# Optimization experiments

Measured on AMD Instinct MI355X. Metric: run time of the kernel, lower is better.

The kernel has to match this reference:

```python
import jax, jax.numpy as jnp
import numpy as np

B, T, C, H, W = 4, 5, 512, 32, 32   # bt = B*T = 20
G = 32                              # GroupNorm groups
EPS = 1e-6


def group_norm(x, gamma, beta):
    # x: [N, C, H, W]; normalize per (group-channels, H, W)
    n, c, h, w = x.shape
    xg = x.reshape(n, G, c // G, h * w)
    mu = jnp.mean(xg, axis=(2, 3), keepdims=True)
    var = jnp.mean((xg - mu) ** 2, axis=(2, 3), keepdims=True)
    xn = ((xg - mu) * jax.lax.rsqrt(var + EPS)).reshape(n, c, h, w)
    return xn * gamma[None, :, None, None] + beta[None, :, None, None]


def conv1x1(x, w, b):
    # 1x1 conv == channel matmul. x: [N,C,H,W], w: [O,C], b: [O]
    return jnp.einsum('nchw,oc->nohw', x, w) + b[None, :, None, None]


def setup_inputs() -> dict:
    key = jax.random.key(0)
    ks = jax.random.split(key, 9)
    inp = {'x': jax.random.normal(ks[0], (B * T, C, H, W), jnp.float32)}
    for i, nm in enumerate(['wq', 'wk', 'wv', 'wo', 'wqt', 'wkt', 'wvt', 'wot']):
        inp[nm] = jax.random.normal(ks[i + 1], (C, C), jnp.float32) * 0.02
        inp['b' + nm[1:]] = jnp.zeros((C,), jnp.float32)
    inp['gamma_s'] = jnp.ones((C,), jnp.float32)
    inp['beta_s'] = jnp.zeros((C,), jnp.float32)
    inp['gamma_t'] = jnp.ones((C,), jnp.float32)
    inp['beta_t'] = jnp.zeros((C,), jnp.float32)
    return inp


def reference(x, wq, bq, wk, bk, wv, bv, wo, bo,
              wqt, bqt, wkt, bkt, wvt, bvt, wot, bot,
              gamma_s, beta_s, gamma_t, beta_t):
    scale = float(C) ** -0.5

    # ---- spatial attention (AttnBlock.forward) ----
    hn = group_norm(x, gamma_s, beta_s)
    q = conv1x1(hn, wq, bq).reshape(B * T, C, H * W)
    k = conv1x1(hn, wk, bk).reshape(B * T, C, H * W)
    v = conv1x1(hn, wv, bv).reshape(B * T, C, H * W)
    # scores [bt, hw_q, hw_k], softmax over keys
    att = jax.nn.softmax(jnp.einsum('bcq,bck->bqk', q, k) * scale, axis=2)
    hsp = jnp.einsum('bck,bqk->bcq', v, att).reshape(B * T, C, H, W)
    spatio = x + conv1x1(hsp, wo, bo)

    # ---- temporal attention across t=5 frames per pixel ----
    hn = group_norm(spatio, gamma_t, beta_t)
    q5 = conv1x1(hn, wqt, bqt).reshape(B, T, C, H, W)
    k5 = conv1x1(hn, wkt, bkt).reshape(B, T, C, H, W)
    v5 = conv1x1(hn, wvt, bvt).reshape(B, T, C, H, W)
    # per-pixel [t, t] attention, softmax over key-frame axis s
    att_t = jax.nn.softmax(jnp.einsum('btchw,bschw->bhwts', q5, k5) * scale, axis=-1)
    htp = jnp.einsum('bhwts,bschw->btchw', att_t, v5).reshape(B * T, C, H, W)

    # NOTE: residual is the ORIGINAL x (faithful to the source), not spatio
    return x + conv1x1(htp, wot, bot)
```

## Files before the change

### kernel.cpp

```cpp
#include <hip/hip_runtime.h>
#include <hip/hip_bf16.h>
#include <stdint.h>

typedef unsigned short u16;
typedef __attribute__((ext_vector_type(8))) short bf16x8;
typedef __attribute__((ext_vector_type(4))) float f32x4;

#define DI __device__ __forceinline__

DI float b2f(u16 u) { return __uint_as_float(((uint32_t)u) << 16); }
DI u16 f2b(float f) {
  uint32_t u = __float_as_uint(f);
  u += 0x7fff + ((u >> 16) & 1);
  return (u16)(u >> 16);
}

DI void gld_lds16(const u16* g, u16* l) {
  __builtin_amdgcn_global_load_lds((const __attribute__((address_space(1))) void*)g,
                                   (__attribute__((address_space(3))) void*)l,
                                   16, 0, 0);
}

__global__ __launch_bounds__(256)
void setup_wb(const float* __restrict__ w0, const float* __restrict__ w1,
              const float* __restrict__ w2, const float* __restrict__ w3,
              const float* __restrict__ w4, const float* __restrict__ w5,
              const float* __restrict__ w6, const float* __restrict__ w7,
              const float* __restrict__ b0, const float* __restrict__ b1,
              const float* __restrict__ b2, const float* __restrict__ b3,
              const float* __restrict__ b4, const float* __restrict__ b5,
              const float* __restrict__ b6, const float* __restrict__ b7,
              u16* __restrict__ dst, float* __restrict__ bdst)
{
  if (blockIdx.x >= 1032) {
    const int a = (blockIdx.x - 1032) * 256 + threadIdx.x;
    float acc = 0.f;
    for (int c = 0; c < 512; ++c) acc += w3[a * 512 + c] * b2[c];
    bdst[4096 + a] = acc;
    return;
  }
  if (blockIdx.x >= 1024) {
    const float* bs[8] = {b0, b1, b2, b3, b4, b5, b6, b7};
    const int a = blockIdx.x - 1024;
    const int i = threadIdx.x;
    bdst[a * 512 + i] = bs[a][i];
    bdst[a * 512 + i + 256] = bs[a][i + 256];
    return;
  }
  const float* srcs[8] = {w0, w1, w2, w3, w4, w5, w6, w7};
  const int mat = blockIdx.x >> 7;
  const int i = (((blockIdx.x & 127) << 8) + threadIdx.x) * 8;
  const float* s = srcs[mat];
  float4 a = *(const float4*)(s + i);
  float4 b = *(const float4*)(s + i + 4);
  alignas(16) u16 v[8] = {f2b(a.x), f2b(a.y), f2b(a.z), f2b(a.w),
                          f2b(b.x), f2b(b.y), f2b(b.z), f2b(b.w)};
  *(uint4*)(dst + (long)mat * 262144 + i) = *(const uint4*)v;
  if (mat == 2) {
    const int row = i >> 9, col = i & 511;
#pragma unroll
    for (int j = 0; j < 8; ++j) dst[8 * 262144 + (col + j) * 512 + row] = v[j];
  }
}

template<int OUTF32, int BIASMODE, int RESID, int SMEXP, int COLSCALE>
__global__ __launch_bounds__(256)
void gemm_bt(const u16* __restrict__ A, long sA, long lda,
             const u16* __restrict__ B, long sB, long ldb,
             void* __restrict__ C, long sC,
             const float* __restrict__ bias,
             const float* __restrict__ resid, long sR,
             int N, int K, float alpha, float* __restrict__ stats)
{
  __shared__ u16 lA[2 * 128 * 32];
  __shared__ u16 lB[2 * 128 * 32];
  const int t = threadIdx.x;
  const int lane = t & 63;
  const int wid = t >> 6;

  const int nx = gridDim.x;
  const int bid = blockIdx.y * nx + blockIdx.x;
  const int nper = (nx * gridDim.y) >> 3;
  const int nid = (bid & 7) * nper + (bid >> 3);
  const int m0 = (nid / nx) * 128, n0 = (nid % nx) * 128;

  const long bz = blockIdx.z;
  const u16* Ab = A + bz * sA;
  const u16* Bb = B + bz * sB;

  const int row = t >> 2;
  const int kc  = (((t & 3) ^ ((t >> 3) & 3)) << 3);

  f32x4 acc[4][4];
#pragma unroll
  for (int i = 0; i < 4; ++i)
#pragma unroll
    for (int j = 0; j < 4; ++j) acc[i][j] = (f32x4){0.f, 0.f, 0.f, 0.f};

  const int ml = lane & 15, qd = lane >> 4;
  const int koff = ((qd ^ ((ml >> 1) & 3)) << 3);
  const int wm = (wid >> 1) * 64, wn = (wid & 1) * 64;

  auto stage = [&](int bsel, int k0) {
    const u16* Ap = Ab + (long)(m0 + row) * lda + (k0 + kc);
    const u16* Bp = Bb + (long)(n0 + row) * ldb + (k0 + kc);
    u16* la = lA + bsel * 4096 + wid * 512;
    u16* lb = lB + bsel * 4096 + wid * 512;
    gld_lds16(Ap, la);
    gld_lds16(Ap + 64 * lda, la + 2048);
    gld_lds16(Bp, lb);
    gld_lds16(Bp + 64 * ldb, lb + 2048);
  };

  const int niter = K >> 5;
  stage(0, 0);
  for (int i = 0; i < niter; ++i) {
    __syncthreads();
    if (i + 1 < niter) stage((i + 1) & 1, (i + 1) << 5);
    const u16* la = lA + (i & 1) * 4096;
    const u16* lb = lB + (i & 1) * 4096;
    bf16x8 af[4], bfr[4];
#pragma unroll
    for (int x = 0; x < 4; ++x)
      af[x] = *(const bf16x8*)&la[(wm + x * 16 + ml) * 32 + koff];
#pragma unroll
    for (int y = 0; y < 4; ++y)
      bfr[y] = *(const bf16x8*)&lb[(wn + y * 16 + ml) * 32 + koff];
#pragma unroll
    for (int x = 0; x < 4; ++x)
#pragma unroll
      for (int y = 0; y < 4; ++y)
        acc[x][y] = __builtin_amdgcn_mfma_f32_16x16x32_bf16(af[x], bfr[y], acc[x][y], 0, 0, 0);
  }

  float inv[4];
  if (COLSCALE) {
#pragma unroll
    for (int j = 0; j < 4; ++j)
      inv[j] = 1.f / stats[bz * 1024 + n0 + wn + j * 16 + ml];
  }
  if (SMEXP) {
    float rs[16];
#pragma unroll
    for (int s = 0; s < 16; ++s) rs[s] = 0.f;
#pragma unroll
    for (int i = 0; i < 4; ++i)
#pragma unroll
      for (int j = 0; j < 4; ++j)
#pragma unroll
        for (int r = 0; r < 4; ++r) {
          float e = __expf(acc[i][j][r] * alpha);
          acc[i][j][r] = e;
          rs[i * 4 + r] += e;
        }
#pragma unroll
    for (int m = 1; m < 16; m <<= 1)
#pragma unroll
      for (int s = 0; s < 16; ++s) rs[s] += __shfl_xor(rs[s], m);
    if (ml == 0) {
#pragma unroll
      for (int i = 0; i < 4; ++i)
#pragma unroll
        for (int r = 0; r < 4; ++r)
          atomicAdd(&stats[bz * 1024 + m0 + wm + i * 16 + qd * 4 + r], rs[i * 4 + r]);
    }
  }

  const long cb = bz * sC;
#pragma unroll
  for (int i = 0; i < 4; ++i) {
#pragma unroll
    for (int j = 0; j < 4; ++j) {
#pragma unroll
      for (int r = 0; r < 4; ++r) {
        int rr = m0 + wm + i * 16 + qd * 4 + r;
        int cc = n0 + wn + j * 16 + ml;
        float v = acc[i][j][r];
        if (!SMEXP) v *= alpha;
        if (COLSCALE) v *= inv[j];
        if (BIASMODE == 1) v += bias[rr];
        if (BIASMODE == 2) v += bias[cc];
        long idx = (long)rr * N + cc;
        if (RESID) v += resid[bz * sR + idx];
        if (OUTF32) ((float*)C)[cb + idx] = v;
        else        ((u16*)C)[cb + idx] = f2b(v);
      }
    }
  }
}

template<int OUTF32, int BIASMODE, int RESID>
__global__ __launch_bounds__(512, 2)
void gemm256(const u16* __restrict__ A, long sA, long lda,
             const u16* __restrict__ B, long sB, long ldb,
             void* __restrict__ C, long sC,
             const float* __restrict__ bias,
             const float* __restrict__ resid, long sR,
             int N, int K, float alpha)
{
  __shared__ u16 lA[4 * 8192];
  __shared__ u16 lB[4 * 8192];
  const int t = threadIdx.x;
  const int lane = t & 63, wid = t >> 6;
  const int wr = wid >> 2, wc = wid & 3;
  const int ml = lane & 15, qd = lane >> 4;

  const int nx = gridDim.x;
  const int bid = blockIdx.y * nx + blockIdx.x;
  const int nper = (nx * gridDim.y) >> 3;
  const int nid = (bid & 7) * nper + (bid >> 3);
  const int m0 = (nid / nx) * 256, n0 = (nid % nx) * 256;

  const long bz = blockIdx.z;
  const u16* Ab = A + bz * sA;
  const u16* Bb = B + bz * sB;

  const int sw = ((lane & 3) ^ ((lane >> 3) & 3)) << 3;
  const int srow = wid * 32 + (lane >> 2);
  const u16* ApS = Ab + (long)(m0 + srow) * lda + sw;
  const u16* BpS = Bb + (long)(n0 + srow) * ldb + sw;
  u16* lwA = lA + wid * 1024;
  u16* lwB = lB + wid * 1024;

  f32x4 acc[8][4];
#pragma unroll
  for (int i = 0; i < 8; ++i)
#pragma unroll
    for (int j = 0; j < 4; ++j) acc[i][j] = (f32x4){0.f, 0.f, 0.f, 0.f};

  const int NT = K >> 5;

  auto stageA = [&](int tk) {
    const int bo = (tk & 3) << 13;
    const u16* p = ApS + ((long)tk << 5);
    gld_lds16(p,              lwA + bo);
    gld_lds16(p + (lda << 4), lwA + bo + 512);
  };
  auto stageB = [&](int tk) {
    const int bo = (tk & 3) << 13;
    const u16* p = BpS + ((long)tk << 5);
    gld_lds16(p,              lwB + bo);
    gld_lds16(p + (ldb << 4), lwB + bo + 512);
  };

  const int koff = (qd ^ ((ml >> 1) & 3)) << 3;
  const int rAo = (wr * 128 + ml) * 32 + koff;
  const int rBo = (wc * 64 + ml) * 32 + koff;

  stageA(0); stageB(0); stageA(1); stageB(1); stageA(2); stageB(2);
  asm volatile("s_waitcnt vmcnt(8)" ::: "memory");
  __builtin_amdgcn_s_barrier();
  __builtin_amdgcn_sched_barrier(0);

  for (int tk = 0; tk < NT; ++tk) {
    const int bo = (tk & 3) << 13;
    const u16* pa = lA + bo + rAo;
    const u16* pb = lB + bo + rBo;
    bf16x8 bfr[4], af[4];

#pragma unroll
    for (int n = 0; n < 4; ++n) bfr[n] = *(const bf16x8*)(pb + n * 512);
#pragma unroll
    for (int m = 0; m < 4; ++m) af[m] = *(const bf16x8*)(pa + m * 512);
    if (tk + 3 < NT) stageA(tk + 3);
    __builtin_amdgcn_sched_barrier(0);
    __builtin_amdgcn_s_barrier();
    asm volatile("s_waitcnt lgkmcnt(0)" ::: "memory");
    __builtin_amdgcn_sched_barrier(0);
    __builtin_amdgcn_s_setprio(1);
#pragma unroll
    for (int m = 0; m < 4; ++m)
#pragma unroll
      for (int n = 0; n < 4; ++n)
        acc[m][n] = __builtin_amdgcn_mfma_f32_16x16x32_bf16(af[m], bfr[n], acc[m][n], 0, 0, 0);
    __builtin_amdgcn_s_setprio(0);
    __builtin_amdgcn_sched_barrier(0);
    __builtin_amdgcn_s_barrier();
    __builtin_amdgcn_sched_barrier(0);

#pragma unroll
    for (int m = 0; m < 4; ++m) af[m] = *(const bf16x8*)(pa + (m + 4) * 512);
    if (tk + 3 < NT) stageB(tk + 3);
    __builtin_amdgcn_sched_barrier(0);
    __builtin_amdgcn_s_barrier();
    asm volatile("s_waitcnt lgkmcnt(0)" ::: "memory");
    __builtin_amdgcn_sched_barrier(0);
    __builtin_amdgcn_s_setprio(1);
#pragma unroll
    for (int m = 0; m < 4; ++m)
#pragma unroll
      for (int n = 0; n < 4; ++n)
        acc[m + 4][n] = __builtin_amdgcn_mfma_f32_16x16x32_bf16(af[m], bfr[n], acc[m + 4][n], 0, 0, 0);
    __builtin_amdgcn_s_setprio(0);
    __builtin_amdgcn_sched_barrier(0);

    if (tk < NT - 1) {
      const int rem = NT - 2 - tk;
      if (rem >= 2)      asm volatile("s_waitcnt vmcnt(8)" ::: "memory");
      else if (rem == 1) asm volatile("s_waitcnt vmcnt(4)" ::: "memory");
      else               asm volatile("s_waitcnt vmcnt(0)" ::: "memory");
      __builtin_amdgcn_s_barrier();
      __builtin_amdgcn_sched_barrier(0);
    }
  }

  const long cb = bz * sC;
#pragma unroll
  for (int mt = 0; mt < 8; ++mt) {
#pragma unroll
    for (int nt = 0; nt < 4; ++nt) {
#pragma unroll
      for (int r = 0; r < 4; ++r) {
        int rr = m0 + wr * 128 + mt * 16 + qd * 4 + r;
        int cc = n0 + wc * 64 + nt * 16 + ml;
        float v = acc[mt][nt][r] * alpha;
        if (BIASMODE == 1) v += bias[rr];
        if (BIASMODE == 2) v += bias[cc];
        long idx = (long)rr * N + cc;
        if (RESID) v += resid[bz * sR + idx];
        if (OUTF32) ((float*)C)[cb + idx] = v;
        else        ((u16*)C)[cb + idx] = f2b(v);
      }
    }
  }
}

__global__ __launch_bounds__(256)
void groupnorm_f32(const float* __restrict__ x, const float* __restrict__ gamma,
                   const float* __restrict__ beta, u16* __restrict__ out)
{
  const int C = 512, HW = 1024;
  const int n = blockIdx.x >> 5, g = blockIdx.x & 31;
  const float* xg = x + ((long)n * C + g * 16) * HW;
  const int t = threadIdx.x;
  float s = 0.f, ss = 0.f;
  for (int ch = t; ch < 4096; ch += 256) {
    float4 u = *(const float4*)(xg + ch * 4);
    s += u.x + u.y + u.z + u.w;
    ss += u.x * u.x + u.y * u.y + u.z * u.z + u.w * u.w;
  }
#pragma unroll
  for (int off = 32; off > 0; off >>= 1) { s += __shfl_xor(s, off); ss += __shfl_xor(ss, off); }
  __shared__ float rs[4], rss[4];
  if ((t & 63) == 0) { rs[t >> 6] = s; rss[t >> 6] = ss; }
  __syncthreads();
  s  = rs[0] + rs[1] + rs[2] + rs[3];
  ss = rss[0] + rss[1] + rss[2] + rss[3];
  const float mu = s * (1.f / 16384.f);
  const float var = ss * (1.f / 16384.f) - mu * mu;
  const float rstd = rsqrtf(var + 1e-6f);
  float gm[16], bt[16];
#pragma unroll
  for (int i = 0; i < 16; ++i) {
    float ga = gamma[g * 16 + i];
    gm[i] = ga * rstd;
    bt[i] = beta[g * 16 + i] - mu * ga * rstd;
  }
  for (int p = t; p < 1024; p += 256) {
    alignas(16) u16 vals[16];
#pragma unroll
    for (int i = 0; i < 16; ++i)
      vals[i] = f2b(xg[(long)i * HW + p] * gm[i] + bt[i]);
    u16* dst = out + ((long)n * HW + p) * C + g * 16;
    *(uint4*)dst       = *(const uint4*)&vals[0];
    *(uint4*)(dst + 8) = *(const uint4*)&vals[8];
  }
}

__global__ __launch_bounds__(256)
void groupnorm_resid(const u16* __restrict__ h, const float* __restrict__ x,
                     const float* __restrict__ gamma,
                     const float* __restrict__ beta, u16* __restrict__ out)
{
  const int C = 512, HW = 1024;
  const int n = blockIdx.x >> 5, g = blockIdx.x & 31;
  const long base = ((long)n * C + g * 16) * HW;
  const float* xg = x + base;
  const u16*  hg = h + base;
  const int t = threadIdx.x;
  float s = 0.f, ss = 0.f;
  for (int ch = t; ch < 4096; ch += 256) {
    float4 u = *(const float4*)(xg + ch * 4);
    uint2 hv = *(const uint2*)(hg + ch * 4);
    float h0 = __uint_as_float(hv.x << 16);
    float h1 = __uint_as_float(hv.x & 0xffff0000u);
    float h2 = __uint_as_float(hv.y << 16);
    float h3 = __uint_as_float(hv.y & 0xffff0000u);
    float v0 = u.x + h0, v1 = u.y + h1, v2 = u.z + h2, v3 = u.w + h3;
    s += v0 + v1 + v2 + v3;
    ss += v0 * v0 + v1 * v1 + v2 * v2 + v3 * v3;
  }
#pragma unroll
  for (int off = 32; off > 0; off >>= 1) { s += __shfl_xor(s, off); ss += __shfl_xor(ss, off); }
  __shared__ float rs[4], rss[4];
  if ((t & 63) == 0) { rs[t >> 6] = s; rss[t >> 6] = ss; }
  __syncthreads();
  s  = rs[0] + rs[1] + rs[2] + rs[3];
  ss = rss[0] + rss[1] + rss[2] + rss[3];
  const float mu = s * (1.f / 16384.f);
  const float var = ss * (1.f / 16384.f) - mu * mu;
  const float rstd = rsqrtf(var + 1e-6f);
  float gm[16], bt[16];
#pragma unroll
  for (int i = 0; i < 16; ++i) {
    float ga = gamma[g * 16 + i];
    gm[i] = ga * rstd;
    bt[i] = beta[g * 16 + i] - mu * ga * rstd;
  }
  for (int p = t; p < 1024; p += 256) {
    alignas(16) u16 vals[16];
#pragma unroll
    for (int i = 0; i < 16; ++i)
      vals[i] = f2b((xg[(long)i * HW + p] + b2f(hg[(long)i * HW + p])) * gm[i] + bt[i]);
    u16* dst = out + ((long)n * HW + p) * C + g * 16;
    *(uint4*)dst       = *(const uint4*)&vals[0];
    *(uint4*)(dst + 8) = *(const uint4*)&vals[8];
  }
}

__global__ __launch_bounds__(256)
void temporal_attn(const u16* __restrict__ qkv, u16* __restrict__ htp)
{
  const int t = threadIdx.x;
  const int wv = t >> 6, lane = t & 63;
  const int pix = blockIdx.x * 4 + wv;
  const int b = pix >> 10, p = pix & 1023;
  const long fs = 1024l * 1536;
  const long rowbase = ((long)b * 5 * 1024 + p) * 1536 + lane * 8;

  float qf[5][8], kf[5][8];
#pragma unroll
  for (int f = 0; f < 5; ++f) {
    bf16x8 qv = *(const bf16x8*)(qkv + rowbase + f * fs);
    bf16x8 kv = *(const bf16x8*)(qkv + rowbase + f * fs + 512);
#pragma unroll
    for (int u = 0; u < 8; ++u) { qf[f][u] = b2f((u16)qv[u]); kf[f][u] = b2f((u16)kv[u]); }
  }
  float sc[25];
#pragma unroll
  for (int i = 0; i < 5; ++i)
#pragma unroll
    for (int j = 0; j < 5; ++j) {
      float a = 0.f;
#pragma unroll
      for (int u = 0; u < 8; ++u) a += qf[i][u] * kf[j][u];
      sc[i * 5 + j] = a;
    }
#pragma unroll
  for (int m = 1; m < 64; m <<= 1)
#pragma unroll
    for (int s = 0; s < 25; ++s) sc[s] += __shfl_xor(sc[s], m);

  const float scale = 0.04419417382415922f;
  float att[5][5];
#pragma unroll
  for (int i = 0; i < 5; ++i) {
    float m = sc[i * 5];
#pragma unroll
    for (int j = 1; j < 5; ++j) m = fmaxf(m, sc[i * 5 + j]);
    float ssum = 0.f;
#pragma unroll
    for (int j = 0; j < 5; ++j) { att[i][j] = __expf((sc[i * 5 + j] - m) * scale); ssum += att[i][j]; }
    float inv = 1.f / ssum;
#pragma unroll
    for (int j = 0; j < 5; ++j) att[i][j] *= inv;
  }

  float of[5][8];
#pragma unroll
  for (int i = 0; i < 5; ++i)
#pragma unroll
    for (int u = 0; u < 8; ++u) of[i][u] = 0.f;
#pragma unroll
  for (int s = 0; s < 5; ++s) {
    bf16x8 vvv = *(const bf16x8*)(qkv + rowbase + s * fs + 1024);
#pragma unroll
    for (int u = 0; u < 8; ++u) {
      float vf = b2f((u16)vvv[u]);
#pragma unroll
      for (int i = 0; i < 5; ++i) of[i][u] += att[i][s] * vf;
    }
  }
  const long obase = ((long)b * 5 * 1024 + p) * 512 + lane * 8;
#pragma unroll
  for (int i = 0; i < 5; ++i) {
    alignas(16) u16 ob[8];
#pragma unroll
    for (int u = 0; u < 8; ++u) ob[u] = f2b(of[i][u]);
    *(uint4*)(htp + obase + i * 1024 * 512) = *(const uint4*)ob;
  }
}

extern "C" void kernel_launch(void* const* d_in, const int* in_sizes, int n_in,
                              void* d_out, int out_size, void* d_ws, size_t ws_size,
                              hipStream_t stream)
{
  const float* x   = (const float*)d_in[0];
  const float* wq  = (const float*)d_in[1];
  const float* bq  = (const float*)d_in[2];
  const float* wk  = (const float*)d_in[3];
  const float* bk  = (const float*)d_in[4];
  const float* wv  = (const float*)d_in[5];
  const float* bv  = (const float*)d_in[6];
  const float* wo  = (const float*)d_in[7];
  const float* bo  = (const float*)d_in[8];
  const float* wqt = (const float*)d_in[9];
  const float* bqt = (const float*)d_in[10];
  const float* wkt = (const float*)d_in[11];
  const float* bkt = (const float*)d_in[12];
  const float* wvt = (const float*)d_in[13];
  const float* bvt = (const float*)d_in[14];
  const float* wot = (const float*)d_in[15];
  const float* bot = (const float*)d_in[16];
  const float* gs  = (const float*)d_in[17];
  const float* bs  = (const float*)d_in[18];
  const float* gt  = (const float*)d_in[19];
  const float* btt = (const float*)d_in[20];

  const long U = 20l * 1024 * 512;
  u16* W0 = (u16*)d_ws;
  u16* W1 = W0 + U;
  u16* W3 = W0 + 3 * U;
  u16* W4 = W0 + 4 * U;
  u16* W6 = W0 + 6 * U;
  u16* W7 = W0 + 7 * U;
  u16* Wt = W0 + 8 * U;
  u16* wvT_b = Wt + 8 * 262144;
  u16* Wovs  = Wt + 9 * 262144;
  float* Bf = (float*)(Wt + 10 * 262144);
  float* Stats = Bf + 8192;
  u16* wo_b  = Wt + 3 * 262144;
  u16* wqt_b = Wt + 4 * 262144;
  u16* wot_b = Wt + 7 * 262144;

  const long S  = 524288;
  const long S2 = 1048576;
  const float scale = 0.04419417382415922f;
  dim3 blk(256);
  dim3 blk5(512);

  setup_wb<<<1034, blk, 0, stream>>>(wq, wk, wv, wo, wqt, wkt, wvt, wot,
                                     bq, bk, bv, bo, bqt, bkt, bvt, bot, Wt, Bf);
  hipMemsetAsync(Stats, 0, 20 * 1024 * sizeof(float), stream);

  gemm_bt<0, 0, 0, 0, 0><<<dim3(4, 4, 1), blk, 0, stream>>>(
      wo_b, 0, 512, wvT_b, 0, 512, Wovs, 0, nullptr, nullptr, 0, 512, 512, 1.f, nullptr);

  groupnorm_f32<<<640, blk, 0, stream>>>(x, gs, bs, W0);
  gemm_bt<0, 2, 0, 0, 0><<<dim3(8, 160, 1), blk, 0, stream>>>(
      W0, 0, 512, Wt, 0, 512, W1, 0, Bf, nullptr, 0, 1024, 512, 1.f, nullptr);
  gemm_bt<0, 1, 0, 0, 0><<<dim3(8, 4, 20), blk, 0, stream>>>(
      Wovs, 0, 512, W0, S, 512, W3, S, Bf + 4096, nullptr, 0, 1024, 512, 1.f, nullptr);
  gemm_bt<0, 0, 0, 1, 0><<<dim3(8, 8, 20), blk, 0, stream>>>(
      W1, S2, 1024, W1 + 512, S2, 1024, W4, S2, nullptr, nullptr, 0, 1024, 512, scale, Stats);
  gemm_bt<0, 1, 0, 0, 1><<<dim3(8, 4, 20), blk, 0, stream>>>(
      W3, S, 1024, W4, S2, 1024, W6, S, Bf + 1536, nullptr, 0, 1024, 1024, 1.f, Stats);
  groupnorm_resid<<<640, blk, 0, stream>>>(W6, x, gt, btt, W7);
  gemm256<0, 2, 0><<<dim3(6, 80, 1), blk5, 0, stream>>>(
      W7, 0, 512, wqt_b, 0, 512, W1, 0, Bf + 2048, nullptr, 0, 1536, 512, 1.f);
  temporal_attn<<<1024, blk, 0, stream>>>(W1, W0);
  gemm_bt<1, 1, 1, 0, 0><<<dim3(8, 4, 20), blk, 0, stream>>>(
      wot_b, 0, 512, W0, S, 512, (float*)d_out, S, Bf + 3584, x, S, 1024, 512, 1.f, nullptr);
}
```

Measured before the change: 442.6 us.

## Fold Wo·Wv product and stats zeroing into setup kernel; global block swizzle

```diff
diff --git a/kernel.cpp b/kernel.cpp
--- a/kernel.cpp
+++ b/kernel.cpp
@@ -32,8 +32,32 @@
               const float* __restrict__ b6, const float* __restrict__ b7,
               u16* __restrict__ dst, float* __restrict__ bdst)
 {
+  const int t = threadIdx.x;
+  if (blockIdx.x >= 1098) {
+    bdst[8192 + (blockIdx.x - 1098) * 256 + t] = 0.f;
+    return;
+  }
+  if (blockIdx.x >= 1034) {
+    const int wb = blockIdx.x - 1034;
+    const int a0 = (wb >> 3) * 64, b0 = (wb & 7) * 64;
+    const int row = a0 + (t >> 2);
+    const int bcol = b0 + (t & 3) * 16;
+    float acc[16];
+#pragma unroll
+    for (int i = 0; i < 16; ++i) acc[i] = 0.f;
+    for (int c = 0; c < 512; ++c) {
+      const float woc = w3[row * 512 + c];
+      const float* wvr = w2 + (long)c * 512 + bcol;
+#pragma unroll
+      for (int i = 0; i < 16; ++i) acc[i] += woc * wvr[i];
+    }
+    u16* o = dst + 9 * 262144 + (long)row * 512 + bcol;
+#pragma unroll
+    for (int i = 0; i < 16; ++i) o[i] = f2b(acc[i]);
+    return;
+  }
   if (blockIdx.x >= 1032) {
-    const int a = (blockIdx.x - 1032) * 256 + threadIdx.x;
+    const int a = (blockIdx.x - 1032) * 256 + t;
     float acc = 0.f;
     for (int c = 0; c < 512; ++c) acc += w3[a * 512 + c] * b2[c];
     bdst[4096 + a] = acc;
@@ -42,25 +66,19 @@
   if (blockIdx.x >= 1024) {
     const float* bs[8] = {b0, b1, b2, b3, b4, b5, b6, b7};
     const int a = blockIdx.x - 1024;
-    const int i = threadIdx.x;
-    bdst[a * 512 + i] = bs[a][i];
-    bdst[a * 512 + i + 256] = bs[a][i + 256];
+    bdst[a * 512 + t] = bs[a][t];
+    bdst[a * 512 + t + 256] = bs[a][t + 256];
     return;
   }
   const float* srcs[8] = {w0, w1, w2, w3, w4, w5, w6, w7};
   const int mat = blockIdx.x >> 7;
-  const int i = (((blockIdx.x & 127) << 8) + threadIdx.x) * 8;
+  const int i = (((blockIdx.x & 127) << 8) + t) * 8;
   const float* s = srcs[mat];
   float4 a = *(const float4*)(s + i);
   float4 b = *(const float4*)(s + i + 4);
   alignas(16) u16 v[8] = {f2b(a.x), f2b(a.y), f2b(a.z), f2b(a.w),
                           f2b(b.x), f2b(b.y), f2b(b.z), f2b(b.w)};
   *(uint4*)(dst + (long)mat * 262144 + i) = *(const uint4*)v;
-  if (mat == 2) {
-    const int row = i >> 9, col = i & 511;
-#pragma unroll
-    for (int j = 0; j < 8; ++j) dst[8 * 262144 + (col + j) * 512 + row] = v[j];
-  }
 }
 
 template<int OUTF32, int BIASMODE, int RESID, int SMEXP, int COLSCALE>
@@ -78,13 +96,16 @@
   const int lane = t & 63;
   const int wid = t >> 6;
 
-  const int nx = gridDim.x;
-  const int bid = blockIdx.y * nx + blockIdx.x;
-  const int nper = (nx * gridDim.y) >> 3;
-  const int nid = (bid & 7) * nper + (bid >> 3);
-  const int m0 = (nid / nx) * 128, n0 = (nid % nx) * 128;
-
-  const long bz = blockIdx.z;
+  const uint32_t nx = gridDim.x, ny = gridDim.y;
+  const uint32_t tpz = nx * ny;
+  const uint32_t nblk = tpz * gridDim.z;
+  const uint32_t g = ((uint32_t)blockIdx.z * ny + blockIdx.y) * nx + blockIdx.x;
+  const uint32_t idx = (g & 7u) * (nblk >> 3) + (g >> 3);
+  const uint32_t bz_ = idx / tpz;
+  const uint32_t r   = idx - bz_ * tpz;
+  const int m0 = (int)(r / nx) * 128, n0 = (int)(r % nx) * 128;
+  const long bz = bz_;
+
   const u16* Ab = A + bz * sA;
   const u16* Bb = B + bz * sB;
 
@@ -148,10 +169,10 @@
 #pragma unroll
       for (int j = 0; j < 4; ++j)
 #pragma unroll
-        for (int r = 0; r < 4; ++r) {
-          float e = __expf(acc[i][j][r] * alpha);
-          acc[i][j][r] = e;
-          rs[i * 4 + r] += e;
+        for (int r2 = 0; r2 < 4; ++r2) {
+          float e = __expf(acc[i][j][r2] * alpha);
+          acc[i][j][r2] = e;
+          rs[i * 4 + r2] += e;
         }
 #pragma unroll
     for (int m = 1; m < 16; m <<= 1)
@@ -161,8 +182,8 @@
 #pragma unroll
       for (int i = 0; i < 4; ++i)
 #pragma unroll
-        for (int r = 0; r < 4; ++r)
-          atomicAdd(&stats[bz * 1024 + m0 + wm + i * 16 + qd * 4 + r], rs[i * 4 + r]);
+        for (int r2 = 0; r2 < 4; ++r2)
+          atomicAdd(&stats[bz * 1024 + m0 + wm + i * 16 + qd * 4 + r2], rs[i * 4 + r2]);
     }
   }
 
@@ -172,18 +193,18 @@
 #pragma unroll
     for (int j = 0; j < 4; ++j) {
 #pragma unroll
-      for (int r = 0; r < 4; ++r) {
-        int rr = m0 + wm + i * 16 + qd * 4 + r;
+      for (int r2 = 0; r2 < 4; ++r2) {
+        int rr = m0 + wm + i * 16 + qd * 4 + r2;
         int cc = n0 + wn + j * 16 + ml;
-        float v = acc[i][j][r];
+        float v = acc[i][j][r2];
         if (!SMEXP) v *= alpha;
         if (COLSCALE) v *= inv[j];
         if (BIASMODE == 1) v += bias[rr];
         if (BIASMODE == 2) v += bias[cc];
-        long idx = (long)rr * N + cc;
-        if (RESID) v += resid[bz * sR + idx];
-        if (OUTF32) ((float*)C)[cb + idx] = v;
-        else        ((u16*)C)[cb + idx] = f2b(v);
+        long ix = (long)rr * N + cc;
+        if (RESID) v += resid[bz * sR + ix];
+        if (OUTF32) ((float*)C)[cb + ix] = v;
+        else        ((u16*)C)[cb + ix] = f2b(v);
       }
     }
   }
@@ -525,11 +546,9 @@
   u16* W6 = W0 + 6 * U;
   u16* W7 = W0 + 7 * U;
   u16* Wt = W0 + 8 * U;
-  u16* wvT_b = Wt + 8 * 262144;
   u16* Wovs  = Wt + 9 * 262144;
   float* Bf = (float*)(Wt + 10 * 262144);
   float* Stats = Bf + 8192;
-  u16* wo_b  = Wt + 3 * 262144;
   u16* wqt_b = Wt + 4 * 262144;
   u16* wot_b = Wt + 7 * 262144;
 
@@ -539,12 +558,8 @@
   dim3 blk(256);
   dim3 blk5(512);
 
-  setup_wb<<<1034, blk, 0, stream>>>(wq, wk, wv, wo, wqt, wkt, wvt, wot,
+  setup_wb<<<1178, blk, 0, stream>>>(wq, wk, wv, wo, wqt, wkt, wvt, wot,
                                      bq, bk, bv, bo, bqt, bkt, bvt, bot, Wt, Bf);
-  hipMemsetAsync(Stats, 0, 20 * 1024 * sizeof(float), stream);
-
-  gemm_bt<0, 0, 0, 0, 0><<<dim3(4, 4, 1), blk, 0, stream>>>(
-      wo_b, 0, 512, wvT_b, 0, 512, Wovs, 0, nullptr, nullptr, 0, 512, 512, 1.f, nullptr);
 
   groupnorm_f32<<<640, blk, 0, stream>>>(x, gs, bs, W0);
   gemm_bt<0, 2, 0, 0, 0><<<dim3(8, 160, 1), blk, 0, stream>>>(
```

Result: slower. 528.5 us (+19.4%).
